# Optimization experiments

Measured on AMD Instinct MI355X. Metric: run time of the kernel, lower is better.

Reference implementation:

```python
import jax, jax.numpy as jnp
import numpy as np

N_Q = 8        # qubits
DENC = 3       # encoding entangling layers
DVAR = 3       # variational entangling layers
SEQ = 64
BATCH = 256
D_FEAT = N_Q * (DENC + 2)   # 40, per-token feature dim
D_W = N_Q * (DVAR + 2)      # 40, per-position weight dim


def _rx(t):
    c = jnp.cos(t / 2).astype(jnp.complex64)
    s = (-1j * jnp.sin(t / 2)).astype(jnp.complex64)
    return jnp.stack([jnp.stack([c, s]), jnp.stack([s, c])])


def _ry(t):
    c = jnp.cos(t / 2)
    s = jnp.sin(t / 2)
    return jnp.stack([jnp.stack([c, -s]), jnp.stack([s, c])]).astype(jnp.complex64)


def _apply1(state, U, wire):
    # state: (2,)*N_Q complex; apply 2x2 gate on `wire`
    s = jnp.tensordot(U, state, axes=([1], [wire]))
    return jnp.moveaxis(s, 0, wire)


def _cnot(state, c, t):
    s0 = jnp.take(state, 0, axis=c)
    s1 = jnpp_flip = jnp.take(state, 1, axis=c)
    t2 = t - 1 if t > c else t
    s1 = jnp.flip(s1, axis=t2)  # X on target when control=1
    return jnp.stack([s0, s1], axis=c)


def _circuit(x, w, sign):
    # x: [D_FEAT] encoding angles, w: [D_W] variational angles
    state = jnp.zeros((2,) * N_Q, jnp.complex64).at[(0,) * N_Q].set(1.0)
    idx = 0
    for j in range(N_Q):
        state = _apply1(state, _rx(x[idx]), j)
        state = _apply1(state, _ry(x[idx + 1]), j)
        idx += 2
    for _ in range(DENC):
        for j in range(N_Q):
            state = _cnot(state, j, (j + 1) % N_Q)
        for j in range(N_Q):
            state = _apply1(state, _ry(x[idx]), j)
            idx += 1
    idx = 0
    for j in range(N_Q):
        state = _apply1(state, _rx(w[idx]), j)
        state = _apply1(state, _ry(w[idx + 1]), j)
        idx += 2
    for _ in range(DVAR):
        for j in range(N_Q):
            state = _cnot(state, j, (j + 1) % N_Q)
        for j in range(N_Q):
            state = _apply1(state, _ry(w[idx]), j)
            idx += 1
    probs = (jnp.abs(state) ** 2).astype(jnp.float32)
    return jnp.sum(probs * sign)


# observable sign tables
_Z0 = jnp.array([1.0, -1.0], jnp.float32).reshape((2,) + (1,) * (N_Q - 1))
_ZALL = jnp.array([1.0, -1.0], jnp.float32)
for _ in range(N_Q - 1):
    _ZALL = _ZALL[..., None] * jnp.array([1.0, -1.0], jnp.float32)


def _batched(sign):
    f = lambda xx, ww: _circuit(xx, ww, sign)
    f = jax.vmap(f, in_axes=(0, 0))      # over seq positions (per-position weights)
    return jax.vmap(f, in_axes=(0, None))  # over batch


_qk = _batched(_Z0)
_v = _batched(_ZALL)  # random_op fixed deterministically to Z x Z x ... x Z


def setup_inputs() -> dict:
    key = jax.random.key(0)
    k1, k2, k3, k4 = jax.random.split(key, 4)
    scale = np.float32(np.pi / 4)
    x = jax.random.normal(k1, (BATCH, SEQ, D_FEAT), jnp.float32)
    pQ = scale * (2 * jax.random.normal(k2, (SEQ, D_W), jnp.float32) - 1)
    pK = scale * (2 * jax.random.normal(k3, (SEQ, D_W), jnp.float32) - 1)
    pV = scale * (2 * jax.random.normal(k4, (SEQ, D_W), jnp.float32) - 1)
    return {"x": x, "params_Q": pQ, "params_K": pK, "params_V": pV}


def reference(x, params_Q, params_K, params_V):
    # Per-token quantum circuit sims -> scalar Q, K, V expectations
    Q = _qk(x, params_Q)   # [B, S]
    K = _qk(x, params_K)   # [B, S]
    V = _v(x, params_V)    # [B, S]  (original returns d identical copies of this)
    # Gaussian-kernel attention: alpha[b,i,m] = exp(-(Q_i - K_m)^2)
    alpha = jnp.exp(-(Q[:, :, None] - K[:, None, :]) ** 2)   # [B, S, S]
    w = alpha / jnp.sum(alpha, axis=-1, keepdims=True)
    att = jnp.einsum('bim,bm->bi', w, V)                     # [B, S]
    return x + att[:, :, None]  # broadcast over d (V copies are identical)
```

## Files before the change

### kernel.cpp

```cpp
#include <hip/hip_runtime.h>

#define SEQd 64
#define BATCHd 256
#define DF 40

typedef float f2 __attribute__((ext_vector_type(2)));
typedef __fp16 h2v __attribute__((ext_vector_type(2)));


__device__ __forceinline__ int lane_id() { return threadIdx.x & 63; }

template<int LM>
__device__ __forceinline__ float xch1(float v) {
  if constexpr (LM == 0) {
    return v;
  } else if constexpr (LM == 1 || LM == 2 || LM == 3 || LM == 7 || LM == 15) {
    constexpr int ctrl = (LM == 1) ? 0xB1 : (LM == 2) ? 0x4E : (LM == 3) ? 0x1B
                       : (LM == 7) ? 0x141 : 0x140;
    return __int_as_float(__builtin_amdgcn_mov_dpp(__float_as_int(v), ctrl, 0xF, 0xF, true));
  } else {
    return __int_as_float(__builtin_amdgcn_ds_swizzle(__float_as_int(v), (LM << 10) | 0x1F));
  }
}

template<int LM>
__device__ __forceinline__ f2 xch2(f2 v) {
  if constexpr (LM == 0) return v;
  f2 r; r.x = xch1<LM>(v.x); r.y = xch1<LM>(v.y); return r;
}

__device__ __forceinline__ f2 jrot(f2 v) { f2 r; r.x = -v.y; r.y = v.x; return r; }

template<int M, int SM>
__device__ __forceinline__ void ry16(f2* a, f2 cs, int lam) {
  constexpr int LM = M >> 4, RM = M & 15, SL = SM >> 4, SR = SM & 15;
  const float c = cs.x, s = cs.y;
  float t0;
  if constexpr (SL != 0) t0 = (__popc(lam & SL) & 1) ? s : -s;
  else                   t0 = -s;
#pragma unroll
  for (int k = 0; k < 16; ++k) {
    const int kp = k ^ RM;
    if (kp < k) continue;
    if (kp == k) {
      const f2 b = xch2<LM>(a[k]);
      const float tk = (__builtin_popcount(k & SR) & 1) ? -t0 : t0;
      a[k] = c * a[k] + tk * b;
    } else {
      const f2 b0 = xch2<LM>(a[kp]);
      const f2 b1 = xch2<LM>(a[k]);
      const float tk  = (__builtin_popcount(k  & SR) & 1) ? -t0 : t0;
      const float tkp = (__builtin_popcount(kp & SR) & 1) ? -t0 : t0;
      a[k]  = c * a[k]  + tk  * b0;
      a[kp] = c * a[kp] + tkp * b1;
    }
  }
}

template<int M, int SM>
__device__ __forceinline__ void su2_16(f2* a, float4 q, int lam) {
  constexpr int LM = M >> 4, RM = M & 15, SL = SM >> 4, SR = SM & 15;
  float sb, sc;
  if constexpr (SL != 0) {
    const bool p = (__popc(lam & SL) & 1) != 0;
    sb = p ? -q.y : q.y; sc = p ? -q.z : q.z;
  } else { sb = q.y; sc = q.z; }
#pragma unroll
  for (int k = 0; k < 16; ++k) {
    const int kp = k ^ RM;
    if (kp < k) continue;
    if (kp == k) {
      const f2 B = xch2<LM>(a[k]);
      const bool pk = (__builtin_popcount(k & SR) & 1) != 0;
      const float fb = pk ? -sb : sb, fc = pk ? -sc : sc;
      const f2 A = a[k];
      a[k] = q.x * A - fc * B + fb * jrot(A) - q.w * jrot(B);
    } else {
      const f2 B0 = xch2<LM>(a[kp]);
      const f2 B1 = xch2<LM>(a[k]);
      const bool pk  = (__builtin_popcount(k  & SR) & 1) != 0;
      const bool pkp = (__builtin_popcount(kp & SR) & 1) != 0;
      const float fb0 = pk  ? -sb : sb, fc0 = pk  ? -sc : sc;
      const float fb1 = pkp ? -sb : sb, fc1 = pkp ? -sc : sc;
      const f2 A0 = a[k], A1 = a[kp];
      a[k]  = q.x * A0 - fc0 * B0 + fb0 * jrot(A0) - q.w * jrot(B0);
      a[kp] = q.x * A1 - fc1 * B1 + fb1 * jrot(A1) - q.w * jrot(B1);
    }
  }
}

__device__ __forceinline__ void layers16(f2* a, const float* __restrict__ tabh, int lam) {
  const f2* L = (const f2*)(tabh + 32);
  ry16<0xC0,0x7F>(a, L[0],  lam);
  ry16<0x60,0xC0>(a, L[1],  lam);
  ry16<0x30,0xE0>(a, L[2],  lam);
  ry16<0x18,0xF0>(a, L[3],  lam);
  ry16<0x0C,0xF8>(a, L[4],  lam);
  ry16<0x06,0xFC>(a, L[5],  lam);
  ry16<0x03,0xFE>(a, L[6],  lam);
  ry16<0xC1,0xFF>(a, L[7],  lam);
  ry16<0xA0,0xD5>(a, L[8],  lam);
  ry16<0x50,0xBF>(a, L[9],  lam);
  ry16<0x28,0x5F>(a, L[10], lam);
  ry16<0x14,0xAF>(a, L[11], lam);
  ry16<0x0A,0x57>(a, L[12], lam);
  ry16<0x05,0xAB>(a, L[13], lam);
  ry16<0xC2,0x55>(a, L[14], lam);
  ry16<0x61,0xAA>(a, L[15], lam);
  ry16<0xF0,0x4C>(a, L[16], lam);
  ry16<0x78,0x6A>(a, L[17], lam);
  ry16<0x3C,0x35>(a, L[18], lam);
  ry16<0x1E,0x9A>(a, L[19], lam);
  ry16<0x0F,0xCD>(a, L[20], lam);
  ry16<0xC7,0x66>(a, L[21], lam);
  ry16<0xA3,0x33>(a, L[22], lam);
  ry16<0x91,0x99>(a, L[23], lam);
}

__device__ __forceinline__ void initial16(f2* a, const float4* __restrict__ F, int lam) {
  su2_16<0x80,0x80>(a, F[0], lam);
  su2_16<0x40,0x40>(a, F[1], lam);
  su2_16<0x20,0x20>(a, F[2], lam);
  su2_16<0x10,0x10>(a, F[3], lam);
  su2_16<0x08,0x08>(a, F[4], lam);
  su2_16<0x04,0x04>(a, F[5], lam);
  su2_16<0x02,0x02>(a, F[6], lam);
  su2_16<0x01,0x01>(a, F[7], lam);
}

__device__ __forceinline__ void pinit16(f2* a, const float4* __restrict__ F, int lam) {
  f2 c; c.x = 1.f; c.y = 0.f;
#pragma unroll
  for (int i = 0; i < 4; ++i) {
    const float4 f = F[3 - i];
    const bool bit = ((lam >> i) & 1) != 0;
    const float ur = bit ? f.z : f.x;
    const float ui = bit ? -f.w : f.y;
    f2 n; n.x = c.x * ur - c.y * ui; n.y = c.x * ui + c.y * ur;
    c = n;
  }
  const float4 f7 = F[7], f6 = F[6], f5 = F[5], f4 = F[4];
  f2 w67[4], w45[4];
#pragma unroll
  for (int j = 0; j < 4; ++j) {
    const bool b7 = (j & 1) != 0, b6 = (j & 2) != 0;
    const float a7r = b7 ? f7.z : f7.x, a7i = b7 ? -f7.w : f7.y;
    const float a6r = b6 ? f6.z : f6.x, a6i = b6 ? -f6.w : f6.y;
    w67[j].x = a6r * a7r - a6i * a7i; w67[j].y = a6r * a7i + a6i * a7r;
    const bool b5 = (j & 1) != 0, b4 = (j & 2) != 0;
    const float a5r = b5 ? f5.z : f5.x, a5i = b5 ? -f5.w : f5.y;
    const float a4r = b4 ? f4.z : f4.x, a4i = b4 ? -f4.w : f4.y;
    w45[j].x = a4r * a5r - a4i * a5i; w45[j].y = a4r * a5i + a4i * a5r;
  }
#pragma unroll
  for (int k = 0; k < 16; ++k) {
    const f2 u = w67[k & 3], w = w45[(k >> 2) & 3];
    f2 t; t.x = u.x * w.x - u.y * w.y; t.y = u.x * w.y + u.y * w.x;
    a[k].x = c.x * t.x - c.y * t.y;
    a[k].y = c.x * t.y + c.y * t.x;
  }
}

__device__ __forceinline__ uint32_t packh(f2 v) {
  h2v h = __builtin_amdgcn_cvt_pkrtz(v.x, v.y);
  return __builtin_bit_cast(uint32_t, h);
}
__device__ __forceinline__ f2 unpackh(uint32_t u) {
  h2v h = __builtin_bit_cast(h2v, u);
  f2 r; r.x = (float)h[0]; r.y = (float)h[1]; return r;
}

__device__ __forceinline__ void snap_write16(const f2* a, uint32_t* sn, int lam) {
  int tgt = 0;
  if (lam & 1) tgt ^= 0x33;
  if (lam & 2) tgt ^= 0x66;
  if (lam & 4) tgt ^= 0xCC;
  if (lam & 8) tgt ^= 0x19;
  constexpr int rc[16] = {0x00,0x2B,0x56,0x7D,0xAC,0x87,0xFA,0xD1,
                          0xD9,0xF2,0x8F,0xA4,0x75,0x5E,0x23,0x08};
#pragma unroll
  for (int k = 0; k < 16; ++k) sn[tgt ^ rc[k]] = packh(a[k]);
}

__device__ __forceinline__ void snap_read16(f2* a, const uint32_t* sn, int lam) {
  const uint4* p = (const uint4*)(sn + lam * 16);
#pragma unroll
  for (int q = 0; q < 4; ++q) {
    const uint4 w = p[q];
    a[4*q+0] = unpackh(w.x); a[4*q+1] = unpackh(w.y);
    a[4*q+2] = unpackh(w.z); a[4*q+3] = unpackh(w.w);
  }
}

template<int SM>
__device__ __forceinline__ float expect16(const f2* a, int lam) {
  constexpr int SL = SM >> 4, SR = SM & 15;
  float s0 = 0.f, s1 = 0.f;
#pragma unroll
  for (int k = 0; k < 16; ++k) {
    const float p = a[k].x * a[k].x + a[k].y * a[k].y;
    if ((__builtin_popcount(k & SR) & 1) != 0) s1 += p; else s0 += p;
  }
  const float d = s0 - s1;
  float v = (__popc(lam & SL) & 1) ? -d : d;
  v += xch1<1>(v); v += xch1<2>(v); v += xch1<4>(v); v += xch1<8>(v);
  return v;
}

__global__ __launch_bounds__(256) void prep_var(
    const float* __restrict__ pQ, const float* __restrict__ pK,
    const float* __restrict__ pV, float* __restrict__ vtab)
{
  const int t = blockIdx.x * 256 + threadIdx.x;
  if (t >= SEQd * 3 * 32) return;
  const int slot = t & 31;
  const int sh = t >> 5;
  const int h = sh % 3, sp = sh / 3;
  const float* w = ((h == 0) ? pQ : (h == 1) ? pK : pV) + sp * DF;
  float* o = vtab + sh * 80;
  if (slot < 8) {
    float cx, sx, cy, sy;
    __sincosf(w[2 * slot]     * 0.5f, &sx, &cx);
    __sincosf(w[2 * slot + 1] * 0.5f, &sy, &cy);
    ((float4*)o)[slot] = make_float4(cy * cx, sy * sx, sy * cx, cy * sx);
  } else {
    float sn, cn;
    __sincosf(w[16 + (slot - 8)] * 0.5f, &sn, &cn);
    ((float2*)(o + 32))[slot - 8] = make_float2(cn, sn);
  }
}

__global__ __launch_bounds__(256) void qsal_circuits(
    const float* __restrict__ x, const float* __restrict__ vtab,
    float* __restrict__ Qo, float* __restrict__ Ko, float* __restrict__ Vo)
{
  __shared__ __align__(16) float etab[16][80];
  __shared__ __align__(16) uint32_t snap[16][264];
  const int tid  = threadIdx.x;
  const int wid  = tid >> 6, lane = tid & 63, lam = lane & 15;
  const int s     = blockIdx.x & 63;
  const int bbase = (blockIdx.x >> 6) << 4;
  const int ci    = wid * 4 + (lane >> 4);

#pragma unroll
  for (int rep = 0; rep < 3; ++rep) {
    const int aIdx = tid + rep * 256;
    if (aIdx < 640) {
      const int cc = aIdx / 40, idx = aIdx - cc * 40;
      const float ang = x[((size_t)(bbase + cc) * 64 + s) * 40 + idx];
      float sn, cn; __sincosf(ang * 0.5f, &sn, &cn);
      if (idx < 16) {
        const int wire = idx >> 1, isy = idx & 1;
        etab[cc][wire * 4 + isy * 2 + 0] = cn;
        etab[cc][wire * 4 + isy * 2 + 1] = sn;
      } else {
        etab[cc][32 + (idx - 16) * 2 + 0] = cn;
        etab[cc][32 + (idx - 16) * 2 + 1] = sn;
      }
    }
  }
  __syncthreads();
  if (tid < 128) {
    const int cc = tid >> 3, wire = tid & 7;
    float4* q = (float4*)etab[cc];
    const float4 f = q[wire];
    q[wire] = make_float4(f.z * f.x, f.w * f.y, f.w * f.x, f.z * f.y);
  }
  __syncthreads();

  f2 a[16];
  pinit16(a, (const float4*)etab[ci], lam);
  layers16(a, etab[ci], lam);
  snap_write16(a, snap[ci], lam);
  __syncthreads();

  const float* vg = vtab + s * 240;
  float e[3];
#pragma unroll
  for (int h = 0; h < 3; ++h) {
    f2 v[16];
    snap_read16(v, snap[ci], lam);
    const float* th = vg + 80 * h;
    initial16(v, (const float4*)th, lam);
    layers16(v, th, lam);
    e[h] = (h == 2) ? expect16<0x88>(v, lam) : expect16<0x4C>(v, lam);
  }
  if (lam == 0) {
    const int gw = (bbase + ci) * 64 + s;
    Qo[gw] = e[0]; Ko[gw] = e[1]; Vo[gw] = e[2];
  }
}

__global__ __launch_bounds__(256) void qsal_attn(
    const float* __restrict__ x,
    const float* __restrict__ Qv,
    const float* __restrict__ Kv,
    const float* __restrict__ Vv,
    float* __restrict__ out)
{
  const int tid  = threadIdx.x;
  const int wid  = tid >> 6;
  const int lane = tid & 63;
  const int bi   = blockIdx.x * 4 + wid;
  const int b    = bi >> 6;

  const float q = Qv[bi];
  const float k = Kv[b * 64 + lane];
  const float v = Vv[b * 64 + lane];
  const float d = q - k;
  float e  = __expf(-d * d);
  float ev = e * v;
#pragma unroll
  for (int m = 1; m < 64; m <<= 1) {
    e  += __shfl_xor(e,  m, 64);
    ev += __shfl_xor(ev, m, 64);
  }
  const float att = ev / e;

  const size_t row = (size_t)bi * DF;
  if (lane < DF) out[row + lane] = x[row + lane] + att;
}

extern "C" void kernel_launch(void* const* d_in, const int* in_sizes, int n_in,
                              void* d_out, int out_size, void* d_ws, size_t ws_size,
                              hipStream_t stream) {
  const float* x  = (const float*)d_in[0];
  const float* pQ = (const float*)d_in[1];
  const float* pK = (const float*)d_in[2];
  const float* pV = (const float*)d_in[3];
  float* out = (float*)d_out;

  float* Qv   = (float*)d_ws;
  float* Kv   = Qv + BATCHd * SEQd;
  float* Vv   = Kv + BATCHd * SEQd;
  float* vtab = Vv + BATCHd * SEQd;

  prep_var<<<dim3(24), dim3(256), 0, stream>>>(pQ, pK, pV, vtab);
  qsal_circuits<<<dim3(1024), dim3(256), 0, stream>>>(x, vtab, Qv, Kv, Vv);
  qsal_attn<<<dim3(BATCHd * SEQd / 4), dim3(256), 0, stream>>>(x, Qv, Kv, Vv, out);
}
```

Measured before the change: 82.93 us.

## Use 8 lanes per circuit with 32 amplitudes each and split Q/K/V across waves

Each 256-amplitude state now lives on 8 lanes holding 32 amplitudes each, instead of 16 lanes holding 16. That turns more gate pairs into in-register work and drops one cross-lane exchange level. The block now handles 8 circuits, with wave 0 running the encoding and waves 1-3 each running one of the Q/K/V variational circuits in parallel rather than one after another. Gates are rewritten with packed-float FMA. In exchange, register pressure doubles, wave 0 sits idle during the variational phase while waves 1-3 wait on it before, and the grid doubles.

```diff
diff --git a/kernel.cpp b/kernel.cpp
--- a/kernel.cpp
+++ b/kernel.cpp
@@ -7,16 +7,14 @@
 typedef float f2 __attribute__((ext_vector_type(2)));
 typedef __fp16 h2v __attribute__((ext_vector_type(2)));
 
-
-__device__ __forceinline__ int lane_id() { return threadIdx.x & 63; }
 
 template<int LM>
 __device__ __forceinline__ float xch1(float v) {
   if constexpr (LM == 0) {
     return v;
-  } else if constexpr (LM == 1 || LM == 2 || LM == 3 || LM == 7 || LM == 15) {
+  } else if constexpr (LM == 1 || LM == 2 || LM == 3 || LM == 7) {
     constexpr int ctrl = (LM == 1) ? 0xB1 : (LM == 2) ? 0x4E : (LM == 3) ? 0x1B
-                       : (LM == 7) ? 0x141 : 0x140;
+                       : 0x141;
     return __int_as_float(__builtin_amdgcn_mov_dpp(__float_as_int(v), ctrl, 0xF, 0xF, true));
   } else {
     return __int_as_float(__builtin_amdgcn_ds_swizzle(__float_as_int(v), (LM << 10) | 0x1F));
@@ -29,136 +27,139 @@
   f2 r; r.x = xch1<LM>(v.x); r.y = xch1<LM>(v.y); return r;
 }
 
-__device__ __forceinline__ f2 jrot(f2 v) { f2 r; r.x = -v.y; r.y = v.x; return r; }
+__device__ __forceinline__ f2 ff(f2 x, f2 y, f2 z) { return __builtin_elementwise_fma(x, y, z); }
+__device__ __forceinline__ f2 cmul(f2 a, f2 b) {
+  f2 r; r.x = a.x * b.x - a.y * b.y; r.y = a.x * b.y + a.y * b.x; return r;
+}
+__device__ __forceinline__ f2 uget(float4 f, bool bit) {
+  f2 r; r.x = bit ? f.z : f.x; r.y = bit ? -f.w : f.y; return r;
+}
 
 template<int M, int SM>
-__device__ __forceinline__ void ry16(f2* a, f2 cs, int lam) {
-  constexpr int LM = M >> 4, RM = M & 15, SL = SM >> 4, SR = SM & 15;
-  const float c = cs.x, s = cs.y;
+__device__ __forceinline__ void ry32(f2* a, f2 cs, int lam) {
+  constexpr int LM = M & 7, RM = M >> 3, SL = SM & 7, SR = SM >> 3;
   float t0;
-  if constexpr (SL != 0) t0 = (__popc(lam & SL) & 1) ? s : -s;
-  else                   t0 = -s;
-#pragma unroll
-  for (int k = 0; k < 16; ++k) {
+  if constexpr (SL != 0) t0 = (__popc(lam & SL) & 1) ? cs.y : -cs.y;
+  else                   t0 = -cs.y;
+  const f2 cv = {cs.x, cs.x};
+  const f2 tp = {t0, t0}, tn = {-t0, -t0};
+#pragma unroll
+  for (int k = 0; k < 32; ++k) {
     const int kp = k ^ RM;
     if (kp < k) continue;
     if (kp == k) {
       const f2 b = xch2<LM>(a[k]);
-      const float tk = (__builtin_popcount(k & SR) & 1) ? -t0 : t0;
-      a[k] = c * a[k] + tk * b;
+      a[k] = ff(b, (__builtin_popcount(k & SR) & 1) ? tn : tp, a[k] * cv);
     } else {
       const f2 b0 = xch2<LM>(a[kp]);
       const f2 b1 = xch2<LM>(a[k]);
-      const float tk  = (__builtin_popcount(k  & SR) & 1) ? -t0 : t0;
-      const float tkp = (__builtin_popcount(kp & SR) & 1) ? -t0 : t0;
-      a[k]  = c * a[k]  + tk  * b0;
-      a[kp] = c * a[kp] + tkp * b1;
+      const f2 t_k  = (__builtin_popcount(k  & SR) & 1) ? tn : tp;
+      const f2 t_kp = (__builtin_popcount(kp & SR) & 1) ? tn : tp;
+      a[k]  = ff(b0, t_k,  a[k]  * cv);
+      a[kp] = ff(b1, t_kp, a[kp] * cv);
     }
   }
 }
 
 template<int M, int SM>
-__device__ __forceinline__ void su2_16(f2* a, float4 q, int lam) {
-  constexpr int LM = M >> 4, RM = M & 15, SL = SM >> 4, SR = SM & 15;
+__device__ __forceinline__ void su2_32(f2* a, float4 q, int lam) {
+  constexpr int LM = M & 7, RM = M >> 3, SL = SM & 7, SR = SM >> 3;
   float sb, sc;
   if constexpr (SL != 0) {
     const bool p = (__popc(lam & SL) & 1) != 0;
     sb = p ? -q.y : q.y; sc = p ? -q.z : q.z;
   } else { sb = q.y; sc = q.z; }
-#pragma unroll
-  for (int k = 0; k < 16; ++k) {
+  const f2 vqa = {q.x, q.x};
+  const f2 vqw = {q.w, -q.w};
+  const f2 vfc0 = {-sc, -sc}, vfb0 = {-sb, sb};
+  const f2 vfc1 = { sc,  sc}, vfb1 = { sb, -sb};
+#pragma unroll
+  for (int k = 0; k < 32; ++k) {
     const int kp = k ^ RM;
     if (kp < k) continue;
     if (kp == k) {
       const f2 B = xch2<LM>(a[k]);
       const bool pk = (__builtin_popcount(k & SR) & 1) != 0;
-      const float fb = pk ? -sb : sb, fc = pk ? -sc : sc;
       const f2 A = a[k];
-      a[k] = q.x * A - fc * B + fb * jrot(A) - q.w * jrot(B);
+      f2 r = A * vqa;
+      r = ff(B, pk ? vfc1 : vfc0, r);
+      r = ff(A.yx, pk ? vfb1 : vfb0, r);
+      r = ff(B.yx, vqw, r);
+      a[k] = r;
     } else {
       const f2 B0 = xch2<LM>(a[kp]);
       const f2 B1 = xch2<LM>(a[k]);
-      const bool pk  = (__builtin_popcount(k  & SR) & 1) != 0;
-      const bool pkp = (__builtin_popcount(kp & SR) & 1) != 0;
-      const float fb0 = pk  ? -sb : sb, fc0 = pk  ? -sc : sc;
-      const float fb1 = pkp ? -sb : sb, fc1 = pkp ? -sc : sc;
+      const bool pk0 = (__builtin_popcount(k  & SR) & 1) != 0;
+      const bool pk1 = (__builtin_popcount(kp & SR) & 1) != 0;
       const f2 A0 = a[k], A1 = a[kp];
-      a[k]  = q.x * A0 - fc0 * B0 + fb0 * jrot(A0) - q.w * jrot(B0);
-      a[kp] = q.x * A1 - fc1 * B1 + fb1 * jrot(A1) - q.w * jrot(B1);
+      f2 r0 = A0 * vqa;
+      r0 = ff(B0, pk0 ? vfc1 : vfc0, r0);
+      r0 = ff(A0.yx, pk0 ? vfb1 : vfb0, r0);
+      r0 = ff(B0.yx, vqw, r0);
+      a[k] = r0;
+      f2 r1 = A1 * vqa;
+      r1 = ff(B1, pk1 ? vfc1 : vfc0, r1);
+      r1 = ff(A1.yx, pk1 ? vfb1 : vfb0, r1);
+      r1 = ff(B1.yx, vqw, r1);
+      a[kp] = r1;
     }
   }
 }
 
-__device__ __forceinline__ void layers16(f2* a, const float* __restrict__ tabh, int lam) {
-  const f2* L = (const f2*)(tabh + 32);
-  ry16<0xC0,0x7F>(a, L[0],  lam);
-  ry16<0x60,0xC0>(a, L[1],  lam);
-  ry16<0x30,0xE0>(a, L[2],  lam);
-  ry16<0x18,0xF0>(a, L[3],  lam);
-  ry16<0x0C,0xF8>(a, L[4],  lam);
-  ry16<0x06,0xFC>(a, L[5],  lam);
-  ry16<0x03,0xFE>(a, L[6],  lam);
-  ry16<0xC1,0xFF>(a, L[7],  lam);
-  ry16<0xA0,0xD5>(a, L[8],  lam);
-  ry16<0x50,0xBF>(a, L[9],  lam);
-  ry16<0x28,0x5F>(a, L[10], lam);
-  ry16<0x14,0xAF>(a, L[11], lam);
-  ry16<0x0A,0x57>(a, L[12], lam);
-  ry16<0x05,0xAB>(a, L[13], lam);
-  ry16<0xC2,0x55>(a, L[14], lam);
-  ry16<0x61,0xAA>(a, L[15], lam);
-  ry16<0xF0,0x4C>(a, L[16], lam);
-  ry16<0x78,0x6A>(a, L[17], lam);
-  ry16<0x3C,0x35>(a, L[18], lam);
-  ry16<0x1E,0x9A>(a, L[19], lam);
-  ry16<0x0F,0xCD>(a, L[20], lam);
-  ry16<0xC7,0x66>(a, L[21], lam);
-  ry16<0xA3,0x33>(a, L[22], lam);
-  ry16<0x91,0x99>(a, L[23], lam);
-}
-
-__device__ __forceinline__ void initial16(f2* a, const float4* __restrict__ F, int lam) {
-  su2_16<0x80,0x80>(a, F[0], lam);
-  su2_16<0x40,0x40>(a, F[1], lam);
-  su2_16<0x20,0x20>(a, F[2], lam);
-  su2_16<0x10,0x10>(a, F[3], lam);
-  su2_16<0x08,0x08>(a, F[4], lam);
-  su2_16<0x04,0x04>(a, F[5], lam);
-  su2_16<0x02,0x02>(a, F[6], lam);
-  su2_16<0x01,0x01>(a, F[7], lam);
-}
-
-__device__ __forceinline__ void pinit16(f2* a, const float4* __restrict__ F, int lam) {
-  f2 c; c.x = 1.f; c.y = 0.f;
-#pragma unroll
-  for (int i = 0; i < 4; ++i) {
-    const float4 f = F[3 - i];
-    const bool bit = ((lam >> i) & 1) != 0;
-    const float ur = bit ? f.z : f.x;
-    const float ui = bit ? -f.w : f.y;
-    f2 n; n.x = c.x * ur - c.y * ui; n.y = c.x * ui + c.y * ur;
-    c = n;
-  }
-  const float4 f7 = F[7], f6 = F[6], f5 = F[5], f4 = F[4];
-  f2 w67[4], w45[4];
-#pragma unroll
-  for (int j = 0; j < 4; ++j) {
-    const bool b7 = (j & 1) != 0, b6 = (j & 2) != 0;
-    const float a7r = b7 ? f7.z : f7.x, a7i = b7 ? -f7.w : f7.y;
-    const float a6r = b6 ? f6.z : f6.x, a6i = b6 ? -f6.w : f6.y;
-    w67[j].x = a6r * a7r - a6i * a7i; w67[j].y = a6r * a7i + a6i * a7r;
-    const bool b5 = (j & 1) != 0, b4 = (j & 2) != 0;
-    const float a5r = b5 ? f5.z : f5.x, a5i = b5 ? -f5.w : f5.y;
-    const float a4r = b4 ? f4.z : f4.x, a4i = b4 ? -f4.w : f4.y;
-    w45[j].x = a4r * a5r - a4i * a5i; w45[j].y = a4r * a5i + a4i * a5r;
-  }
-#pragma unroll
-  for (int k = 0; k < 16; ++k) {
-    const f2 u = w67[k & 3], w = w45[(k >> 2) & 3];
-    f2 t; t.x = u.x * w.x - u.y * w.y; t.y = u.x * w.y + u.y * w.x;
-    a[k].x = c.x * t.x - c.y * t.y;
-    a[k].y = c.x * t.y + c.y * t.x;
-  }
+__device__ __forceinline__ void layers32(f2* a, const f2* __restrict__ L, int lam) {
+  ry32<0xC0,0x7F>(a, L[0],  lam);
+  ry32<0x60,0xC0>(a, L[1],  lam);
+  ry32<0x30,0xE0>(a, L[2],  lam);
+  ry32<0x18,0xF0>(a, L[3],  lam);
+  ry32<0x0C,0xF8>(a, L[4],  lam);
+  ry32<0x06,0xFC>(a, L[5],  lam);
+  ry32<0x03,0xFE>(a, L[6],  lam);
+  ry32<0xC1,0xFF>(a, L[7],  lam);
+  ry32<0xA0,0xD5>(a, L[8],  lam);
+  ry32<0x50,0xBF>(a, L[9],  lam);
+  ry32<0x28,0x5F>(a, L[10], lam);
+  ry32<0x14,0xAF>(a, L[11], lam);
+  ry32<0x0A,0x57>(a, L[12], lam);
+  ry32<0x05,0xAB>(a, L[13], lam);
+  ry32<0xC2,0x55>(a, L[14], lam);
+  ry32<0x61,0xAA>(a, L[15], lam);
+  ry32<0xF0,0x4C>(a, L[16], lam);
+  ry32<0x78,0x6A>(a, L[17], lam);
+  ry32<0x3C,0x35>(a, L[18], lam);
+  ry32<0x1E,0x9A>(a, L[19], lam);
+  ry32<0x0F,0xCD>(a, L[20], lam);
+  ry32<0xC7,0x66>(a, L[21], lam);
+  ry32<0xA3,0x33>(a, L[22], lam);
+  ry32<0x91,0x99>(a, L[23], lam);
+}
+
+__device__ __forceinline__ void initial32(f2* a, const float4* __restrict__ F, int lam) {
+  su2_32<0x80,0x80>(a, F[0], lam);
+  su2_32<0x40,0x40>(a, F[1], lam);
+  su2_32<0x20,0x20>(a, F[2], lam);
+  su2_32<0x10,0x10>(a, F[3], lam);
+  su2_32<0x08,0x08>(a, F[4], lam);
+  su2_32<0x04,0x04>(a, F[5], lam);
+  su2_32<0x02,0x02>(a, F[6], lam);
+  su2_32<0x01,0x01>(a, F[7], lam);
+}
+
+__device__ __forceinline__ void pinit32(f2* a, const float4* __restrict__ F, int lam) {
+  f2 c = {1.f, 0.f};
+#pragma unroll
+  for (int i = 0; i < 3; ++i)
+    c = cmul(c, uget(F[7 - i], ((lam >> i) & 1) != 0));
+  f2 wlo[4], whi[8];
+#pragma unroll
+  for (int t = 0; t < 4; ++t)
+    wlo[t] = cmul(uget(F[4], (t & 1) != 0), uget(F[3], ((t >> 1) & 1) != 0));
+#pragma unroll
+  for (int t = 0; t < 8; ++t)
+    whi[t] = cmul(cmul(uget(F[2], (t & 1) != 0), uget(F[1], ((t >> 1) & 1) != 0)),
+                  uget(F[0], ((t >> 2) & 1) != 0));
+#pragma unroll
+  for (int k = 0; k < 32; ++k)
+    a[k] = cmul(cmul(c, wlo[k & 3]), whi[k >> 2]);
 }
 
 __device__ __forceinline__ uint32_t packh(f2 v) {
@@ -170,40 +171,44 @@
   f2 r; r.x = (float)h[0]; r.y = (float)h[1]; return r;
 }
 
-__device__ __forceinline__ void snap_write16(const f2* a, uint32_t* sn, int lam) {
+__device__ __forceinline__ void snap_write32(const f2* a, uint32_t* sn, int lam) {
   int tgt = 0;
-  if (lam & 1) tgt ^= 0x33;
-  if (lam & 2) tgt ^= 0x66;
-  if (lam & 4) tgt ^= 0xCC;
-  if (lam & 8) tgt ^= 0x19;
-  constexpr int rc[16] = {0x00,0x2B,0x56,0x7D,0xAC,0x87,0xFA,0xD1,
-                          0xD9,0xF2,0x8F,0xA4,0x75,0x5E,0x23,0x08};
-#pragma unroll
-  for (int k = 0; k < 16; ++k) sn[tgt ^ rc[k]] = packh(a[k]);
-}
-
-__device__ __forceinline__ void snap_read16(f2* a, const uint32_t* sn, int lam) {
-  const uint4* p = (const uint4*)(sn + lam * 16);
-#pragma unroll
-  for (int q = 0; q < 4; ++q) {
-    const uint4 w = p[q];
-    a[4*q+0] = unpackh(w.x); a[4*q+1] = unpackh(w.y);
-    a[4*q+2] = unpackh(w.z); a[4*q+3] = unpackh(w.w);
+  if (lam & 1) tgt ^= 0x2B;
+  if (lam & 2) tgt ^= 0x56;
+  if (lam & 4) tgt ^= 0xAC;
+#pragma unroll
+  for (int k = 0; k < 32; ++k) {
+    const int rck = ((k & 1) ? 0xD9 : 0) ^ ((k & 2) ? 0x33 : 0) ^ ((k & 4) ? 0x66 : 0)
+                  ^ ((k & 8) ? 0xCC : 0) ^ ((k & 16) ? 0x19 : 0);
+    const int qq = tgt ^ rck;
+    sn[((qq & 7) << 5) | (qq >> 3)] = packh(a[k]);
+  }
+}
+
+__device__ __forceinline__ void snap_read32(f2* a, const uint32_t* sn, int lam) {
+  const uint4* p = (const uint4*)(sn + lam * 32);
+#pragma unroll
+  for (int t = 0; t < 8; ++t) {
+    const uint4 w = p[t];
+    a[4*t+0] = unpackh(w.x); a[4*t+1] = unpackh(w.y);
+    a[4*t+2] = unpackh(w.z); a[4*t+3] = unpackh(w.w);
   }
 }
 
 template<int SM>
-__device__ __forceinline__ float expect16(const f2* a, int lam) {
-  constexpr int SL = SM >> 4, SR = SM & 15;
+__device__ __forceinline__ float expect32(const f2* a, int lam) {
+  constexpr int SL = SM & 7, SR = SM >> 3;
   float s0 = 0.f, s1 = 0.f;
 #pragma unroll
-  for (int k = 0; k < 16; ++k) {
+  for (int k = 0; k < 32; ++k) {
     const float p = a[k].x * a[k].x + a[k].y * a[k].y;
     if ((__builtin_popcount(k & SR) & 1) != 0) s1 += p; else s0 += p;
   }
   const float d = s0 - s1;
-  float v = (__popc(lam & SL) & 1) ? -d : d;
-  v += xch1<1>(v); v += xch1<2>(v); v += xch1<4>(v); v += xch1<8>(v);
+  float v;
+  if constexpr (SL != 0) v = (__popc(lam & SL) & 1) ? -d : d;
+  else                   v = d;
+  v += xch1<1>(v); v += xch1<2>(v); v += xch1<4>(v);
   return v;
 }
 
@@ -234,60 +239,56 @@
     const float* __restrict__ x, const float* __restrict__ vtab,
     float* __restrict__ Qo, float* __restrict__ Ko, float* __restrict__ Vo)
 {
-  __shared__ __align__(16) float etab[16][80];
-  __shared__ __align__(16) uint32_t snap[16][264];
-  const int tid  = threadIdx.x;
-  const int wid  = tid >> 6, lane = tid & 63, lam = lane & 15;
-  const int s     = blockIdx.x & 63;
-  const int bbase = (blockIdx.x >> 6) << 4;
-  const int ci    = wid * 4 + (lane >> 4);
-
-#pragma unroll
-  for (int rep = 0; rep < 3; ++rep) {
-    const int aIdx = tid + rep * 256;
-    if (aIdx < 640) {
-      const int cc = aIdx / 40, idx = aIdx - cc * 40;
-      const float ang = x[((size_t)(bbase + cc) * 64 + s) * 40 + idx];
-      float sn, cn; __sincosf(ang * 0.5f, &sn, &cn);
-      if (idx < 16) {
-        const int wire = idx >> 1, isy = idx & 1;
-        etab[cc][wire * 4 + isy * 2 + 0] = cn;
-        etab[cc][wire * 4 + isy * 2 + 1] = sn;
-      } else {
-        etab[cc][32 + (idx - 16) * 2 + 0] = cn;
-        etab[cc][32 + (idx - 16) * 2 + 1] = sn;
-      }
+  __shared__ __align__(16) float etab[8][84];
+  __shared__ __align__(16) uint32_t snap[8][264];
+  const int tid = threadIdx.x;
+  const int wid = tid >> 6, lane = tid & 63;
+  const int ci = lane >> 3, lam = lane & 7;
+  const int s = blockIdx.x & 63;
+  const int bbase = (blockIdx.x >> 6) << 3;
+
+  for (int t = tid; t < 320; t += 256) {
+    const int cc = t / 40, idx = t - cc * 40;
+    const float ang = x[((size_t)(bbase + cc) * 64 + s) * 40 + idx];
+    float sn, cn; __sincosf(ang * 0.5f, &sn, &cn);
+    if (idx < 16) {
+      const int wire = idx >> 1, isy = idx & 1;
+      etab[cc][wire * 4 + isy * 2 + 0] = cn;
+      etab[cc][wire * 4 + isy * 2 + 1] = sn;
+    } else {
+      etab[cc][32 + (idx - 16) * 2 + 0] = cn;
+      etab[cc][32 + (idx - 16) * 2 + 1] = sn;
     }
   }
   __syncthreads();
-  if (tid < 128) {
+  if (tid < 64) {
     const int cc = tid >> 3, wire = tid & 7;
-    float4* q = (float4*)etab[cc];
-    const float4 f = q[wire];
-    q[wire] = make_float4(f.z * f.x, f.w * f.y, f.w * f.x, f.z * f.y);
+    float4* qt = (float4*)etab[cc];
+    const float4 f = qt[wire];
+    qt[wire] = make_float4(f.z * f.x, f.w * f.y, f.w * f.x, f.z * f.y);
   }
   __syncthreads();
 
-  f2 a[16];
-  pinit16(a, (const float4*)etab[ci], lam);
-  layers16(a, etab[ci], lam);
-  snap_write16(a, snap[ci], lam);
+  if (wid == 0) {
+    f2 a[32];
+    pinit32(a, (const float4*)etab[ci], lam);
+    layers32(a, (const f2*)(etab[ci] + 32), lam);
+    snap_write32(a, snap[ci], lam);
+  }
   __syncthreads();
 
-  const float* vg = vtab + s * 240;
-  float e[3];
-#pragma unroll
-  for (int h = 0; h < 3; ++h) {
-    f2 v[16];
-    snap_read16(v, snap[ci], lam);
-    const float* th = vg + 80 * h;
-    initial16(v, (const float4*)th, lam);
-    layers16(v, th, lam);
-    e[h] = (h == 2) ? expect16<0x88>(v, lam) : expect16<0x4C>(v, lam);
-  }
-  if (lam == 0) {
-    const int gw = (bbase + ci) * 64 + s;
-    Qo[gw] = e[0]; Ko[gw] = e[1]; Vo[gw] = e[2];
+  if (wid >= 1) {
+    const int h = wid - 1;
+    const float* th = vtab + s * 240 + 80 * h;
+    f2 v[32];
+    snap_read32(v, snap[ci], lam);
+    initial32(v, (const float4*)th, lam);
+    layers32(v, (const f2*)(th + 32), lam);
+    const float e = (h == 2) ? expect32<0x88>(v, lam) : expect32<0x4C>(v, lam);
+    if (lam == 0) {
+      float* op = (h == 0) ? Qo : (h == 1) ? Ko : Vo;
+      op[(bbase + ci) * 64 + s] = e;
+    }
   }
 }
 
@@ -336,6 +337,6 @@
   float* vtab = Vv + BATCHd * SEQd;
 
   prep_var<<<dim3(24), dim3(256), 0, stream>>>(pQ, pK, pV, vtab);
-  qsal_circuits<<<dim3(1024), dim3(256), 0, stream>>>(x, vtab, Qv, Kv, Vv);
+  qsal_circuits<<<dim3(2048), dim3(256), 0, stream>>>(x, vtab, Qv, Kv, Vv);
   qsal_attn<<<dim3(BATCHd * SEQd / 4), dim3(256), 0, stream>>>(x, Qv, Kv, Vv, out);
 }
```

Result: slower. 90.17 us (+8.7%).
